# Kernel tuning notes

Hardware: AMD Instinct MI355X
Metric: run time of the kernel (lower is better)

The kernel has to match this reference:

```python
import jax, jax.numpy as jnp
import numpy as np

N_EMBD = 1024
N_HEAD = 16
HEAD_SIZE = N_EMBD // N_HEAD  # 64

def setup_inputs() -> dict:
    key = jax.random.key(0)
    ks = jax.random.split(key, 6)
    B, T, C, H, S = 2, 2048, N_EMBD, N_HEAD, HEAD_SIZE
    sc = 1.0 / np.sqrt(C)
    x = jax.random.normal(ks[0], (B, T, C), dtype=jnp.float32)
    # stacked per-head projection weights (no bias), [H, C, S]
    Wq = jax.random.normal(ks[1], (H, C, S), dtype=jnp.float32) * sc
    Wk = jax.random.normal(ks[2], (H, C, S), dtype=jnp.float32) * sc
    Wv = jax.random.normal(ks[3], (H, C, S), dtype=jnp.float32) * sc
    Wp = jax.random.normal(ks[4], (C, C), dtype=jnp.float32) * sc
    bp = jax.random.normal(ks[5], (C,), dtype=jnp.float32) * 0.01
    return {"x": x, "Wq": Wq, "Wk": Wk, "Wv": Wv, "Wp": Wp, "bp": bp}

def reference(x, Wq, Wk, Wv, Wp, bp):
    # Eval-mode forward (dropout = identity), default non-flash path.
    B, T, C = x.shape
    H, _, S = Wq.shape
    q = jnp.einsum('btc,hcs->bhts', x, Wq)
    k = jnp.einsum('btc,hcs->bhts', x, Wk)
    v = jnp.einsum('btc,hcs->bhts', x, Wv)
    att = jnp.einsum('bhts,bhus->bhtu', q, k) * (1.0 / np.sqrt(S))
    causal = jnp.tril(jnp.ones((T, T), dtype=bool))
    att = jnp.where(causal[None, None], att, -jnp.inf)
    att = jax.nn.softmax(att, axis=-1)
    y = jnp.einsum('bhtu,bhus->bhts', att, v)
    # concat heads along feature dim (head-major), then output projection
    y = y.transpose(0, 2, 1, 3).reshape(B, T, H * S)
    return y @ Wp.T + bp
```

## Files before the change

kernel.cpp:

```cpp
#include <hip/hip_runtime.h>
#include <hip/hip_bf16.h>
#include <cmath>

typedef __attribute__((ext_vector_type(8))) short bf16x8;
typedef __attribute__((ext_vector_type(4))) float f32x4;
typedef __attribute__((ext_vector_type(16))) float f32x16;

__device__ __forceinline__ unsigned short f2bf(float f) {
    union { float f; unsigned int i; } c; c.f = f;
    unsigned int i = c.i;
    unsigned int r = i + 0x7FFF + ((i >> 16) & 1);
    return (unsigned short)(r >> 16);
}

__device__ __forceinline__ float fast_exp2(float x) {
    float r;
    asm("v_exp_f32 %0, %1" : "=v"(r) : "v"(x));
    return r;
}

__device__ __forceinline__ void gload_lds16(const unsigned short* g, unsigned short* l) {
    __builtin_amdgcn_global_load_lds((const __attribute__((address_space(1))) unsigned int*)g,
                                     (__attribute__((address_space(3))) unsigned int*)l, 16, 0, 0);
}

__global__ void k_cvt_all(const float* __restrict__ x, const float* __restrict__ Wp,
                          const float* __restrict__ Wq, const float* __restrict__ Wk,
                          const float* __restrict__ Wv,
                          unsigned short* __restrict__ x_bf, unsigned short* __restrict__ Wp_bf,
                          unsigned short* __restrict__ Wt) {
    __shared__ unsigned short lt[64][72];
    int bid = blockIdx.x;
    int t = threadIdx.x;
    if (bid < 5120) {
        const float* src = (bid < 4096) ? x : Wp;
        unsigned short* dst = (bid < 4096) ? x_bf : Wp_bf;
        int i = ((bid < 4096) ? bid : (bid - 4096)) * 256 + t;
        float4 v = reinterpret_cast<const float4*>(src)[i];
        ushort4 o;
        o.x = f2bf(v.x); o.y = f2bf(v.y); o.z = f2bf(v.z); o.w = f2bf(v.w);
        reinterpret_cast<ushort4*>(dst)[i] = o;
        return;
    }
    int sub = bid - 5120;
    int ct  = sub & 15;
    int h   = (sub >> 4) & 15;
    int sec = sub >> 8;
    const float* W = (sec == 0) ? Wq : ((sec == 1) ? Wk : Wv);
    float sc = (sec == 0) ? 0.1803368801f : 1.0f;
    #pragma unroll
    for (int q = 0; q < 4; q++) {
        int id = t + q * 256;
        int c  = id >> 4;
        int s4 = (id & 15) * 4;
        float4 v = *reinterpret_cast<const float4*>(&W[((size_t)(h * 1024) + (ct * 64 + c)) * 64 + s4]);
        lt[s4 + 0][c] = f2bf(v.x * sc);
        lt[s4 + 1][c] = f2bf(v.y * sc);
        lt[s4 + 2][c] = f2bf(v.z * sc);
        lt[s4 + 3][c] = f2bf(v.w * sc);
    }
    __syncthreads();
    #pragma unroll
    for (int q = 0; q < 2; q++) {
        int id = t + q * 256;
        int s  = id >> 3;
        int c8 = (id & 7) * 8;
        bf16x8 val = *reinterpret_cast<const bf16x8*>(&lt[s][c8]);
        int n = sec * 1024 + h * 64 + s;
        *reinterpret_cast<bf16x8*>(&Wt[(size_t)n * 1024 + ct * 64 + c8]) = val;
    }
}

__launch_bounds__(256, 4)
__global__ void k_gemm_qkv(const unsigned short* __restrict__ x_bf,
                           const unsigned short* __restrict__ Wt,
                           unsigned short* __restrict__ q_nat,
                           unsigned short* __restrict__ k_nat,
                           unsigned short* __restrict__ vT) {
    __shared__ unsigned short Asm[2][128][32];
    __shared__ unsigned short Bsm[2][128][32];
    const int K = 1024;
    int cpx = gridDim.x >> 3;
    int bid = (blockIdx.x & 7) * cpx + (blockIdx.x >> 3);
    bool isV = (bid >= 512);
    const unsigned short* A;
    const unsigned short* Bt;
    int m0, n0;
    if (!isV) {
        n0 = (bid & 15) << 7;
        m0 = (bid >> 4) << 7;
        A = x_bf; Bt = Wt;
    } else {
        int vb = bid - 512;
        n0 = (vb & 31) << 7;
        m0 = (vb >> 5) << 7;
        A = Wt + (size_t)2048 * 1024;
        Bt = x_bf;
    }
    int t = threadIdx.x;
    int lane = t & 63, w = t >> 6;
    int wr = w >> 1, wc = w & 1;
    int l15 = lane & 15, lg = lane >> 4;
    int srow = lane >> 2;
    int scol = ((lane & 3) ^ ((lane >> 3) & 3)) << 3;

    f32x4 acc[4][4];
    #pragma unroll
    for (int i = 0; i < 4; i++)
        #pragma unroll
        for (int j = 0; j < 4; j++) acc[i][j] = (f32x4){0.f, 0.f, 0.f, 0.f};

    auto STAGE = [&](int kt, int buf) {
        #pragma unroll
        for (int q = 0; q < 2; q++) {
            int rb = q * 64 + w * 16;
            int row = rb + srow;
            gload_lds16(&A[(size_t)(m0 + row) * K + kt + scol], &Asm[buf][rb][0]);
            gload_lds16(&Bt[(size_t)(n0 + row) * K + kt + scol], &Bsm[buf][rb][0]);
        }
    };

    const int NT = K >> 5;
    STAGE(0, 0);
    asm volatile("s_waitcnt vmcnt(0)" ::: "memory");
    __builtin_amdgcn_s_barrier();
    int cur = 0;

    for (int tt = 0; tt < NT; tt++) {
        if (tt + 1 < NT) STAGE((tt + 1) << 5, cur ^ 1);

        bf16x8 af[4], bfr[4];
        int xg = (l15 >> 1) & 3;
        #pragma unroll
        for (int mi = 0; mi < 4; mi++) {
            int row = wr * 64 + mi * 16 + l15;
            af[mi] = *reinterpret_cast<const bf16x8*>((const char*)&Asm[cur][row][0] + ((lg ^ xg) << 4));
        }
        #pragma unroll
        for (int nj = 0; nj < 4; nj++) {
            int row = wc * 64 + nj * 16 + l15;
            bfr[nj] = *reinterpret_cast<const bf16x8*>((const char*)&Bsm[cur][row][0] + ((lg ^ xg) << 4));
        }
        asm volatile("s_waitcnt lgkmcnt(0)" ::: "memory");
        __builtin_amdgcn_sched_barrier(0);
        __builtin_amdgcn_s_setprio(1);
        #pragma unroll
        for (int mi = 0; mi < 4; mi++)
            #pragma unroll
            for (int nj = 0; nj < 4; nj++)
                acc[mi][nj] = __builtin_amdgcn_mfma_f32_16x16x32_bf16(af[mi], bfr[nj], acc[mi][nj], 0, 0, 0);
        __builtin_amdgcn_s_setprio(0);

        asm volatile("s_waitcnt vmcnt(0)" ::: "memory");
        __builtin_amdgcn_s_barrier();
        cur ^= 1;
    }

    unsigned short* qkdst = nullptr;
    int noff = 0;
    if (!isV) { qkdst = (n0 < 1024) ? q_nat : k_nat; noff = (n0 < 1024) ? 0 : 1024; }
    #pragma unroll
    for (int mi = 0; mi < 4; mi++) {
        #pragma unroll
        for (int nj = 0; nj < 4; nj++) {
            #pragma unroll
            for (int r = 0; r < 4; r++) {
                int m = m0 + wr * 64 + mi * 16 + lg * 4 + r;
                int n = n0 + wc * 64 + nj * 16 + l15;
                float v = acc[mi][nj][r];
                if (!isV) {
                    qkdst[(size_t)m * 1024 + (n - noff)] = f2bf(v);
                } else {
                    int bb = n >> 11, ttn = n & 2047;
                    int hh = m >> 6, ss = m & 63;
                    vT[(((size_t)(bb * 16 + hh)) * 64 + ss) * 2048 + ttn] = f2bf(v);
                }
            }
        }
    }
}

__launch_bounds__(512, 4)
__global__ void k_attn(const unsigned short* __restrict__ q_nat,
                       const unsigned short* __restrict__ k_nat,
                       const unsigned short* __restrict__ vT,
                       unsigned short* __restrict__ y_bf) {
    __shared__ __align__(16) unsigned short SM[2][2][64][64];
    __shared__ float clB[128];
    const int T = 2048, H = 16;
    int bid = blockIdx.x;
    int bh = bid & 31;
    int g  = bid >> 5;
    int p  = (g < 8) ? (15 - g) : (g - 8);
    int h = bh & 15, b = bh >> 4;
    int t = threadIdx.x;
    int lane = t & 63, w = t >> 6;
    int pr = w >> 2, rg = w & 3;
    int l31 = lane & 31, hi = lane >> 5;
    int q0 = p << 7;
    int warp_q0 = q0 + rg * 32;
    int qg = warp_q0 + l31;
    int jmax = 2 * p + 1;

    const unsigned short* kbase = k_nat + (size_t)(b * T) * 1024 + h * 64;
    const unsigned short* vbase = vT + ((size_t)(b * H + h) * 64) * 2048;

    int sxor = ((lane & 7) ^ (lane >> 3)) << 3;

    auto STAGE = [&](int j) {
        #pragma unroll
        for (int r = 0; r < 2; r++) {
            int rb = r * 32 + rg * 8;
            int grow = rb + (lane >> 3);
            gload_lds16(kbase + (size_t)(j * 64 + grow) * 1024 + sxor, &SM[0][pr][rb][0]);
            gload_lds16(vbase + (size_t)grow * 2048 + j * 64 + sxor, &SM[1][pr][rb][0]);
        }
    };

    bf16x8 qf[4];
    #pragma unroll
    for (int tt = 0; tt < 4; tt++)
        qf[tt] = *reinterpret_cast<const bf16x8*>(
            q_nat + (size_t)(b * T + qg) * 1024 + h * 64 + tt * 16 + hi * 8);

    bf16x8 ones;
    #pragma unroll
    for (int z = 0; z < 8; z++) ones[z] = (short)0x3F80;

    f32x16 acc0, acc1, lacc;
    #pragma unroll
    for (int r = 0; r < 16; r++) { acc0[r] = 0.f; acc1[r] = 0.f; lacc[r] = 0.f; }

    if (pr == 0) STAGE(0);
    __syncthreads();

    for (int k = 0; k <= jmax; k++) {
        bool iCompute = (pr == (k & 1));
        if (!iCompute) {
            if (k + 1 <= jmax) STAGE(k + 1);
        } else {
            const char* kb = (const char*)&SM[0][pr][0][0];
            const char* vb = (const char*)&SM[1][pr][0][0];
            int rsw = (l31 & 7) << 4;
            int j = k;

            f32x16 s0, s1;
            #pragma unroll
            for (int r = 0; r < 16; r++) { s0[r] = 0.f; s1[r] = 0.f; }
            __builtin_amdgcn_s_setprio(1);
            #pragma unroll
            for (int tt = 0; tt < 4; tt++) {
                int cb = (tt * 32 + hi * 16) ^ rsw;
                bf16x8 kf0 = *reinterpret_cast<const bf16x8*>(kb + l31 * 128 + cb);
                bf16x8 kf1 = *reinterpret_cast<const bf16x8*>(kb + (32 + l31) * 128 + cb);
                s0 = __builtin_amdgcn_mfma_f32_32x32x16_bf16(kf0, qf[tt], s0, 0, 0, 0);
                s1 = __builtin_amdgcn_mfma_f32_32x32x16_bf16(kf1, qf[tt], s1, 0, 0, 0);
            }
            __builtin_amdgcn_s_setprio(0);

            if (j * 64 + 63 > warp_q0) {
                #pragma unroll
                for (int r = 0; r < 16; r++) {
                    int kvr = (r & 3) + 8 * (r >> 2) + 4 * hi + j * 64;
                    if (kvr > qg) s0[r] = -INFINITY;
                    if (kvr + 32 > qg) s1[r] = -INFINITY;
                }
            }

            #pragma unroll
            for (int r = 0; r < 16; r++) {
                s0[r] = fast_exp2(s0[r]);
                s1[r] = fast_exp2(s1[r]);
            }

            unsigned int c[16];
            #pragma unroll
            for (int i2 = 0; i2 < 8; i2++) {
                asm("v_cvt_pk_bf16_f32 %0, %1, %2" : "=v"(c[i2]) : "v"(s0[2 * i2]), "v"(s0[2 * i2 + 1]));
                asm("v_cvt_pk_bf16_f32 %0, %1, %2" : "=v"(c[8 + i2]) : "v"(s1[2 * i2]), "v"(s1[2 * i2 + 1]));
            }
            bf16x8 pa[4];
            #pragma unroll
            for (int ks = 0; ks < 4; ks++) {
                unsigned int clo0 = c[ks * 4 + 0], clo1 = c[ks * 4 + 1];
                unsigned int chi0 = c[ks * 4 + 2], chi1 = c[ks * 4 + 3];
                unsigned int pl0 = (unsigned int)__shfl_xor((int)clo0, 32, 64);
                unsigned int pl1 = (unsigned int)__shfl_xor((int)clo1, 32, 64);
                unsigned int ph0 = (unsigned int)__shfl_xor((int)chi0, 32, 64);
                unsigned int ph1 = (unsigned int)__shfl_xor((int)chi1, 32, 64);
                union { unsigned int u[4]; bf16x8 v; } fr;
                fr.u[0] = hi ? ph0 : clo0;
                fr.u[1] = hi ? ph1 : clo1;
                fr.u[2] = hi ? chi0 : pl0;
                fr.u[3] = hi ? chi1 : pl1;
                pa[ks] = fr.v;
            }

            __builtin_amdgcn_s_setprio(1);
            #pragma unroll
            for (int ks = 0; ks < 4; ks++) {
                int cb = (ks * 32 + hi * 16) ^ rsw;
                bf16x8 v0 = *reinterpret_cast<const bf16x8*>(vb + l31 * 128 + cb);
                bf16x8 v1 = *reinterpret_cast<const bf16x8*>(vb + (32 + l31) * 128 + cb);
                acc0 = __builtin_amdgcn_mfma_f32_32x32x16_bf16(pa[ks], v0, acc0, 0, 0, 0);
                acc1 = __builtin_amdgcn_mfma_f32_32x32x16_bf16(pa[ks], v1, acc1, 0, 0, 0);
                lacc = __builtin_amdgcn_mfma_f32_32x32x16_bf16(pa[ks], ones, lacc, 0, 0, 0);
            }
            __builtin_amdgcn_s_setprio(0);
        }

        __syncthreads();
    }

    float* Ocomb = (float*)&SM[0][0][0][0];
    if (pr == 1) {
        #pragma unroll
        for (int r = 0; r < 16; r++) {
            int qr = (r & 3) + 8 * (r >> 2) + 4 * hi;
            int rr = rg * 32 + qr;
            Ocomb[rr * 64 + l31] = acc0[r];
            Ocomb[rr * 64 + 32 + l31] = acc1[r];
            if (l31 == 0) clB[rr] = lacc[r];
        }
    }
    __syncthreads();
    if (pr == 0) {
        #pragma unroll
        for (int r = 0; r < 16; r++) {
            int qr = (r & 3) + 8 * (r >> 2) + 4 * hi;
            int rr = rg * 32 + qr;
            float lt2 = lacc[r] + clB[rr];
            float dv = 1.0f / lt2;
            float o0 = acc0[r] + Ocomb[rr * 64 + l31];
            float o1 = acc1[r] + Ocomb[rr * 64 + 32 + l31];
            size_t row = (size_t)(b * T + q0 + rr) * 1024 + h * 64;
            y_bf[row + l31] = f2bf(o0 * dv);
            y_bf[row + 32 + l31] = f2bf(o1 * dv);
        }
    }
}

__launch_bounds__(256, 2)
__global__ void k_gemm_proj(const unsigned short* __restrict__ A,
                            const unsigned short* __restrict__ Bt,
                            float* __restrict__ out, const float* __restrict__ bp) {
    __shared__ unsigned short Asm[2][128][64];
    __shared__ unsigned short Bsm[2][64][64];
    const int K = 1024, nb = 16;
    int cpx = gridDim.x >> 3;
    int bid = (blockIdx.x & 7) * cpx + (blockIdx.x >> 3);
    int n0 = (bid % nb) << 6;
    int m0 = (bid / nb) << 7;
    int t = threadIdx.x;
    int lane = t & 63, w = t >> 6;
    int wr = w >> 1, wc = w & 1;
    int l15 = lane & 15, lg = lane >> 4;
    int sr = lane >> 3;
    int scol = ((lane & 7) ^ sr) << 3;

    f32x4 acc[4][2];
    #pragma unroll
    for (int i = 0; i < 4; i++)
        #pragma unroll
        for (int j = 0; j < 2; j++) acc[i][j] = (f32x4){0.f, 0.f, 0.f, 0.f};

    auto STAGE = [&](int kt, int buf) {
        #pragma unroll
        for (int q = 0; q < 4; q++) {
            int rb = q * 32 + w * 8;
            gload_lds16(&A[(size_t)(m0 + rb + sr) * K + kt + scol], &Asm[buf][rb][0]);
        }
        #pragma unroll
        for (int q = 0; q < 2; q++) {
            int rb = q * 32 + w * 8;
            gload_lds16(&Bt[(size_t)(n0 + rb + sr) * K + kt + scol], &Bsm[buf][rb][0]);
        }
    };

    const int NT = K >> 6;
    STAGE(0, 0);
    asm volatile("s_waitcnt vmcnt(0)" ::: "memory");
    __builtin_amdgcn_s_barrier();
    int cur = 0;

    for (int tt = 0; tt < NT; tt++) {
        if (tt + 1 < NT) STAGE((tt + 1) << 6, cur ^ 1);
        bf16x8 af[4][2], bfr[2][2];
        int x15 = (l15 & 7) << 3;
        #pragma unroll
        for (int mi = 0; mi < 4; mi++) {
            int row = wr * 64 + mi * 16 + l15;
            af[mi][0] = *reinterpret_cast<const bf16x8*>(&Asm[cur][row][(lg * 8) ^ x15]);
            af[mi][1] = *reinterpret_cast<const bf16x8*>(&Asm[cur][row][(32 + lg * 8) ^ x15]);
        }
        #pragma unroll
        for (int nj = 0; nj < 2; nj++) {
            int row = wc * 32 + nj * 16 + l15;
            bfr[nj][0] = *reinterpret_cast<const bf16x8*>(&Bsm[cur][row][(lg * 8) ^ x15]);
            bfr[nj][1] = *reinterpret_cast<const bf16x8*>(&Bsm[cur][row][(32 + lg * 8) ^ x15]);
        }
        asm volatile("s_waitcnt lgkmcnt(0)" ::: "memory");
        __builtin_amdgcn_sched_barrier(0);
        __builtin_amdgcn_s_setprio(1);
        #pragma unroll
        for (int mi = 0; mi < 4; mi++)
            #pragma unroll
            for (int nj = 0; nj < 2; nj++) {
                acc[mi][nj] = __builtin_amdgcn_mfma_f32_16x16x32_bf16(af[mi][0], bfr[nj][0], acc[mi][nj], 0, 0, 0);
                acc[mi][nj] = __builtin_amdgcn_mfma_f32_16x16x32_bf16(af[mi][1], bfr[nj][1], acc[mi][nj], 0, 0, 0);
            }
        __builtin_amdgcn_s_setprio(0);
        asm volatile("s_waitcnt vmcnt(0)" ::: "memory");
        __builtin_amdgcn_s_barrier();
        cur ^= 1;
    }

    #pragma unroll
    for (int mi = 0; mi < 4; mi++)
        #pragma unroll
        for (int nj = 0; nj < 2; nj++)
            #pragma unroll
            for (int r = 0; r < 4; r++) {
                int m = m0 + wr * 64 + mi * 16 + lg * 4 + r;
                int n = n0 + wc * 32 + nj * 16 + l15;
                out[(size_t)m * 1024 + n] = acc[mi][nj][r] + bp[n];
            }
}

extern "C" void kernel_launch(void* const* d_in, const int* in_sizes, int n_in,
                              void* d_out, int out_size, void* d_ws, size_t ws_size,
                              hipStream_t stream) {
    const float* x  = (const float*)d_in[0];
    const float* Wq = (const float*)d_in[1];
    const float* Wk = (const float*)d_in[2];
    const float* Wv = (const float*)d_in[3];
    const float* Wp = (const float*)d_in[4];
    const float* bp = (const float*)d_in[5];
    float* out = (float*)d_out;

    char* ws = (char*)d_ws;
    unsigned short* x_bf  = (unsigned short*)(ws);
    unsigned short* Wt    = (unsigned short*)(ws + ((size_t)8  << 20));
    unsigned short* Wp_bf = (unsigned short*)(ws + ((size_t)14 << 20));
    unsigned short* q_nat = (unsigned short*)(ws + ((size_t)16 << 20));
    unsigned short* k_nat = (unsigned short*)(ws + ((size_t)24 << 20));
    unsigned short* vT    = (unsigned short*)(ws + ((size_t)32 << 20));
    unsigned short* y_bf  = (unsigned short*)(ws + ((size_t)40 << 20));

    k_cvt_all<<<5888, 256, 0, stream>>>(x, Wp, Wq, Wk, Wv, x_bf, Wp_bf, Wt);
    k_gemm_qkv<<<768, 256, 0, stream>>>(x_bf, Wt, q_nat, k_nat, vT);
    k_attn<<<512, 512, 0, stream>>>(q_nat, k_nat, vT, y_bf);
    k_gemm_proj<<<512, 256, 0, stream>>>(y_bf, Wp_bf, out, bp);
}
```

Before: 100.1 us.

## Split attention KV range across two blocks and combine partials in a normalize kernel

Each (batch, head, query-tile) attention block is split into two blocks, each covering half of the causal KV tiles. Both write unnormalized bf16 partial outputs and per-row softmax denominators into reused workspace buffers. A new elementwise kernel sums the partials, divides by the summed denominators and writes the projection input. The aim is to double grid parallelism and even out per-block causal work. The cost is an extra launch, extra global traffic for the partial outputs, and extra bf16 rounding of the unnormalized partials.

```diff
diff --git a/kernel.cpp b/kernel.cpp
--- a/kernel.cpp
+++ b/kernel.cpp
@@ -11,6 +11,11 @@
     unsigned int i = c.i;
     unsigned int r = i + 0x7FFF + ((i >> 16) & 1);
     return (unsigned short)(r >> 16);
+}
+
+__device__ __forceinline__ float bf2f(unsigned short u) {
+    union { unsigned int i; float f; } c; c.i = ((unsigned int)u) << 16;
+    return c.f;
 }
 
 __device__ __forceinline__ float fast_exp2(float x) {
@@ -184,14 +189,17 @@
 __global__ void k_attn(const unsigned short* __restrict__ q_nat,
                        const unsigned short* __restrict__ k_nat,
                        const unsigned short* __restrict__ vT,
-                       unsigned short* __restrict__ y_bf) {
+                       unsigned short* __restrict__ Op0, unsigned short* __restrict__ Op1,
+                       float* __restrict__ el0, float* __restrict__ el1) {
     __shared__ __align__(16) unsigned short SM[2][2][64][64];
     __shared__ float clB[128];
     const int T = 2048, H = 16;
     int bid = blockIdx.x;
     int bh = bid & 31;
-    int g  = bid >> 5;
-    int p  = (g < 8) ? (15 - g) : (g - 8);
+    int rest = bid >> 5;
+    int hf = rest >> 4;
+    int rrv = rest & 15;
+    int p = (rrv < 8) ? rrv : (23 - rrv);
     int h = bh & 15, b = bh >> 4;
     int t = threadIdx.x;
     int lane = t & 63, w = t >> 6;
@@ -200,20 +208,21 @@
     int q0 = p << 7;
     int warp_q0 = q0 + rg * 32;
     int qg = warp_q0 + l31;
-    int jmax = 2 * p + 1;
+    int jbase = hf * (p + 1);
+    int jmaxL = p;
 
     const unsigned short* kbase = k_nat + (size_t)(b * T) * 1024 + h * 64;
     const unsigned short* vbase = vT + ((size_t)(b * H + h) * 64) * 2048;
 
     int sxor = ((lane & 7) ^ (lane >> 3)) << 3;
 
-    auto STAGE = [&](int j) {
+    auto STAGE = [&](int jg) {
         #pragma unroll
         for (int r = 0; r < 2; r++) {
             int rb = r * 32 + rg * 8;
             int grow = rb + (lane >> 3);
-            gload_lds16(kbase + (size_t)(j * 64 + grow) * 1024 + sxor, &SM[0][pr][rb][0]);
-            gload_lds16(vbase + (size_t)grow * 2048 + j * 64 + sxor, &SM[1][pr][rb][0]);
+            gload_lds16(kbase + (size_t)(jg * 64 + grow) * 1024 + sxor, &SM[0][pr][rb][0]);
+            gload_lds16(vbase + (size_t)grow * 2048 + jg * 64 + sxor, &SM[1][pr][rb][0]);
         }
     };
 
@@ -231,18 +240,18 @@
     #pragma unroll
     for (int r = 0; r < 16; r++) { acc0[r] = 0.f; acc1[r] = 0.f; lacc[r] = 0.f; }
 
-    if (pr == 0) STAGE(0);
+    if (pr == 0) STAGE(jbase);
     __syncthreads();
 
-    for (int k = 0; k <= jmax; k++) {
+    for (int k = 0; k <= jmaxL; k++) {
         bool iCompute = (pr == (k & 1));
         if (!iCompute) {
-            if (k + 1 <= jmax) STAGE(k + 1);
+            if (k + 1 <= jmaxL) STAGE(jbase + k + 1);
         } else {
             const char* kb = (const char*)&SM[0][pr][0][0];
             const char* vb = (const char*)&SM[1][pr][0][0];
             int rsw = (l31 & 7) << 4;
-            int j = k;
+            int j = jbase + k;
 
             f32x16 s0, s1;
             #pragma unroll
@@ -312,6 +321,8 @@
         __syncthreads();
     }
 
+    unsigned short* Opb = hf ? Op1 : Op0;
+    float* elb = hf ? el1 : el0;
     float* Ocomb = (float*)&SM[0][0][0][0];
     if (pr == 1) {
         #pragma unroll
@@ -329,15 +340,35 @@
         for (int r = 0; r < 16; r++) {
             int qr = (r & 3) + 8 * (r >> 2) + 4 * hi;
             int rr = rg * 32 + qr;
-            float lt2 = lacc[r] + clB[rr];
-            float dv = 1.0f / lt2;
             float o0 = acc0[r] + Ocomb[rr * 64 + l31];
             float o1 = acc1[r] + Ocomb[rr * 64 + 32 + l31];
             size_t row = (size_t)(b * T + q0 + rr) * 1024 + h * 64;
-            y_bf[row + l31] = f2bf(o0 * dv);
-            y_bf[row + 32 + l31] = f2bf(o1 * dv);
-        }
-    }
+            Opb[row + l31] = f2bf(o0);
+            Opb[row + 32 + l31] = f2bf(o1);
+            if (l31 == 0) elb[(size_t)(b * 16 + h) * 2048 + q0 + rr] = lacc[r] + clB[rr];
+        }
+    }
+}
+
+__global__ void k_norm(const unsigned short* __restrict__ Op0, const unsigned short* __restrict__ Op1,
+                       const float* __restrict__ el0, const float* __restrict__ el1,
+                       unsigned short* __restrict__ yout) {
+    int i8 = blockIdx.x * 256 + threadIdx.x;
+    size_t e = (size_t)i8 * 8;
+    int bb = i8 >> 18;
+    int trow = (i8 >> 7) & 2047;
+    int h = (i8 & 127) >> 3;
+    size_t li = (size_t)(bb * 16 + h) * 2048 + trow;
+    float rinv = 1.0f / (el0[li] + el1[li]);
+    bf16x8 a = *reinterpret_cast<const bf16x8*>(Op0 + e);
+    bf16x8 bq = *reinterpret_cast<const bf16x8*>(Op1 + e);
+    bf16x8 o;
+    #pragma unroll
+    for (int j = 0; j < 8; j++) {
+        float f = (bf2f((unsigned short)a[j]) + bf2f((unsigned short)bq[j])) * rinv;
+        o[j] = (short)f2bf(f);
+    }
+    *reinterpret_cast<bf16x8*>(yout + e) = o;
 }
 
 __launch_bounds__(256, 2)
@@ -447,8 +478,15 @@
     unsigned short* vT    = (unsigned short*)(ws + ((size_t)32 << 20));
     unsigned short* y_bf  = (unsigned short*)(ws + ((size_t)40 << 20));
 
+    unsigned short* Op0 = x_bf;
+    unsigned short* Op1 = y_bf;
+    float* el0 = (float*)(ws + ((size_t)8 << 20));
+    float* el1 = (float*)(ws + ((size_t)8 << 20) + (512 << 10));
+    unsigned short* yout = q_nat;
+
     k_cvt_all<<<5888, 256, 0, stream>>>(x, Wp, Wq, Wk, Wv, x_bf, Wp_bf, Wt);
     k_gemm_qkv<<<768, 256, 0, stream>>>(x_bf, Wt, q_nat, k_nat, vT);
-    k_attn<<<512, 512, 0, stream>>>(q_nat, k_nat, vT, y_bf);
-    k_gemm_proj<<<512, 256, 0, stream>>>(y_bf, Wp_bf, out, bp);
-}
+    k_attn<<<1024, 512, 0, stream>>>(q_nat, k_nat, vT, Op0, Op1, el0, el1);
+    k_norm<<<2048, 256, 0, stream>>>(Op0, Op1, el0, el1, yout);
+    k_gemm_proj<<<512, 256, 0, stream>>>(yout, Wp_bf, out, bp);
+}
```

New measurement: 110.5 us. 10.4% more time.
